# Optimization experiments

Measured on AMD Instinct MI355X. Metric: run time of the kernel, lower is better.

## Reference

```python
import jax, jax.numpy as jnp
import numpy as np

B, S, D = 32, 1024, 1024
H = 16            # attention heads
T = 8             # num_tasks (probe tokens)
E = 8             # num_experts
K = 2             # top_k
HID = 4 * D       # expert hidden dim
EPS = 1e-5


def setup_inputs() -> dict:
    key = jax.random.key(0)
    ks = jax.random.split(key, 12)
    sd = 1.0 / np.sqrt(D)
    inp = {
        "x": jax.random.normal(ks[0], (B, S, D), jnp.float32),
        "probe": jax.random.normal(ks[1], (1, T, D), jnp.float32) * 0.02,
        "in_proj_w": jax.random.normal(ks[2], (3 * D, D), jnp.float32) * sd,
        "in_proj_b": jnp.zeros((3 * D,), jnp.float32),
        "out_proj_w": jax.random.normal(ks[3], (D, D), jnp.float32) * sd,
        "out_proj_b": jnp.zeros((D,), jnp.float32),
        "ln_gamma": jnp.ones((D,), jnp.float32),
        "ln_beta": jnp.zeros((D,), jnp.float32),
        "gate_w": jax.random.normal(ks[4], (T, D, E), jnp.float32) * sd,  # per-task gate (task-aware)
        "w1": jax.random.normal(ks[5], (E, D, HID), jnp.float32) * sd,
        "b1": jnp.zeros((E, HID), jnp.float32),
        "w2": jax.random.normal(ks[6], (E, HID, D), jnp.float32) / np.sqrt(HID),
        "b2": jnp.zeros((E, D), jnp.float32),
    }
    return inp


def reference(x, probe, in_proj_w, in_proj_b, out_proj_w, out_proj_b,
              ln_gamma, ln_beta, gate_w, w1, b1, w2, b2):
    b, s, d = x.shape
    t = probe.shape[1]
    dh = d // H
    # --- multihead cross attention: query = probe, key/value = x ---
    wq, wk, wv = in_proj_w[:d], in_proj_w[d:2 * d], in_proj_w[2 * d:]
    bq, bk, bv = in_proj_b[:d], in_proj_b[d:2 * d], in_proj_b[2 * d:]
    q = jnp.broadcast_to(probe, (b, t, d)) @ wq.T + bq           # [B,T,D]
    k = x @ wk.T + bk                                            # [B,S,D]
    v = x @ wv.T + bv
    q = q.reshape(b, t, H, dh).transpose(0, 2, 1, 3)             # bhtd
    k = k.reshape(b, s, H, dh).transpose(0, 2, 1, 3)             # bhsd
    v = v.reshape(b, s, H, dh).transpose(0, 2, 1, 3)
    scores = jnp.einsum('bhtd,bhsd->bhts', q, k) / np.sqrt(dh)
    attn = jax.nn.softmax(scores, axis=-1)                       # [B,H,T,S]
    ctx = jnp.einsum('bhts,bhsd->bhtd', attn, v)
    ctx = ctx.transpose(0, 2, 1, 3).reshape(b, t, d)
    attn_out = ctx @ out_proj_w.T + out_proj_b                   # [B,T,D]
    attn_weights = attn.mean(axis=1)                             # torch avg over heads
    # --- layernorm ---
    mu = attn_out.mean(-1, keepdims=True)
    var = attn_out.var(-1, keepdims=True)
    y = (attn_out - mu) * jax.lax.rsqrt(var + EPS) * ln_gamma + ln_beta
    # --- task-aware MoE: per-task gate, top-k routing ---
    logits = jnp.einsum('btd,tde->bte', y, gate_w)               # [B,T,E]
    probs = jax.nn.softmax(logits, axis=-1)
    tok = y.reshape(b * t, d)
    p = probs.reshape(b * t, E)
    topv, topi = jax.lax.top_k(p, K)                             # [N,K]
    wgt = topv / topv.sum(-1, keepdims=True)
    gates = jnp.zeros((b * t, E), y.dtype).at[jnp.arange(b * t)[:, None], topi].set(wgt)
    # all experts on all tokens (N=B*T is small); grouped GEMM form
    h = jax.nn.gelu(jnp.einsum('nd,edh->enh', tok, w1) + b1[:, None, :], approximate=False)
    eo = jnp.einsum('enh,ehd->end', h, w2) + b2[:, None, :]      # [E,N,D]
    moe_out = jnp.einsum('ne,end->nd', gates, eo).reshape(b, t, d)
    # load-balancing aux loss
    dispatch = (jax.nn.one_hot(topi, E, dtype=y.dtype)).sum(1)   # [N,E] 0/1
    f = dispatch.mean(0)
    P = p.mean(0)
    moe_loss = E * jnp.sum(f * P)
    final = attn_out + moe_out
    return final, moe_loss, attn_weights
```

## Files before the change

kernel.cpp:

```cpp
#include <hip/hip_runtime.h>
#include <hip/hip_bf16.h>
#include <math.h>


using bf16x8  = __attribute__((ext_vector_type(8))) short;
using f32x4   = __attribute__((ext_vector_type(4))) float;
using short4v = __attribute__((ext_vector_type(4))) short;

__device__ inline short f2bf(float f) {
  unsigned u = __builtin_bit_cast(unsigned, f);
  u = (u + 0x7fffu + ((u >> 16) & 1u)) >> 16;
  return (short)u;
}
__device__ inline int bswz(int k, int n) {
  return (((k >> 3) ^ ((n >> 2) & 3)) << 3) | (k & 7);
}

#define LGKM0() asm volatile("s_waitcnt lgkmcnt(0)" ::: "memory")
#define RAWBAR() do { __builtin_amdgcn_s_barrier(); __builtin_amdgcn_sched_barrier(0); } while (0)

static constexpr long OFF_Q       = 0;
static constexpr long OFF_QWB     = 8192;
static constexpr long OFF_QB      = 73728;
static constexpr long OFF_PSUM    = 73856;
static constexpr long OFF_FCNT    = 73864;
static constexpr long OFF_GATES   = 73872;
static constexpr long OFF_CTX     = 75920;
static constexpr long OFF_ATTNOUT = 338064;
static constexpr long OFF_EO      = 600208;
static constexpr long OFF_CTXP    = 2697360;
static constexpr long OFF_AOP     = 3745936;
static constexpr long OFF_SCORES  = 4794512;
static constexpr long OFF_AXP     = 8988816;
static constexpr long OFF_YB      = 17377424;
static constexpr long OFF_HB      = 17508496;

__global__ __launch_bounds__(256) void compute_q_k(const float* __restrict__ probe,
                                                   const float* __restrict__ in_w,
                                                   const float* __restrict__ in_b,
                                                   float* __restrict__ q) {
  int wid = threadIdx.x >> 6, lane = threadIdx.x & 63;
  int idx = blockIdx.x * 4 + wid;
  int t = idx >> 10, d = idx & 1023;
  const float* pr = probe + (long)t * 1024;
  const float* wr = in_w + (long)d * 1024;
  float s = 0.f;
  for (int k = lane * 4; k < 1024; k += 256) {
    float4 a = *(const float4*)&pr[k];
    float4 b = *(const float4*)&wr[k];
    s += a.x * b.x + a.y * b.y + a.z * b.z + a.w * b.w;
  }
  for (int o = 32; o; o >>= 1) s += __shfl_xor(s, o);
  if (!lane) q[idx] = s + in_b[d];
}

__global__ __launch_bounds__(256) void compute_qw_k(const float* __restrict__ q,
                                                    const float* __restrict__ in_w,
                                                    const float* __restrict__ in_b,
                                                    short* __restrict__ qwb,
                                                    float* __restrict__ qb) {
  const int h = blockIdx.y;
  const int tid = threadIdx.x;
  const int d = blockIdx.x * 256 + tid;
  __shared__ float qh[8][64];
  if (tid < 64) {
#pragma unroll
    for (int t = 0; t < 8; ++t) qh[t][tid] = q[t * 1024 + h * 64 + tid] * 0.125f;
  }
  __syncthreads();
  const float* wk = in_w + 1048576 + (long)h * 64 * 1024;
  float acc[8];
#pragma unroll
  for (int t = 0; t < 8; ++t) acc[t] = 0.f;
  for (int j = 0; j < 64; ++j) {
    float w = wk[(long)j * 1024 + d];
#pragma unroll
    for (int t = 0; t < 8; ++t) acc[t] += qh[t][j] * w;
  }
#pragma unroll
  for (int t = 0; t < 8; ++t) qwb[(long)(h * 8 + t) * 1024 + d] = f2bf(acc[t]);
  if (blockIdx.x == 0 && tid < 8) {
    float s = 0.f;
    for (int j = 0; j < 64; ++j) s += qh[tid][j] * in_b[1024 + h * 64 + j];
    qb[h * 8 + tid] = s;
  }
}

__global__ __launch_bounds__(512)
void gemm_sc(const short* __restrict__ qwb, const float* __restrict__ xp,
             float* __restrict__ scores) {
  const int b = blockIdx.z;
  const int n0 = blockIdx.x * 64;
  const float* B = xp + (long)b * 1048576;
  float* C = scores + (long)b * 131072;
  const int tid = threadIdx.x;
  __shared__ short As[128][40], Bs[64][40];

  f32x4 acc[2][2];
#pragma unroll
  for (int i = 0; i < 2; ++i)
#pragma unroll
    for (int j = 0; j < 2; ++j)
#pragma unroll
      for (int qq = 0; qq < 4; ++qq) acc[i][j][qq] = 0.f;

  const int wid = tid >> 6, lane = tid & 63;
  const int wm = wid & 3, wn = wid >> 2;
  const int r = lane & 15, kg = (lane >> 4) * 8;
  const int am = tid >> 2, ak8 = (tid & 3) * 8;
  const int bn = tid >> 3, bk4 = (tid & 7) * 4;

  bf16x8 ra;
  float4 rb;
  auto loadT = [&](int k0) {
    ra = *(const bf16x8*)&qwb[(long)am * 1024 + k0 + ak8];
    rb = *(const float4*)&B[(long)(n0 + bn) * 1024 + k0 + bk4];
  };
  auto storeT = [&]() {
    *(bf16x8*)&As[am][ak8] = ra;
    short4v s;
    s.x = f2bf(rb.x); s.y = f2bf(rb.y); s.z = f2bf(rb.z); s.w = f2bf(rb.w);
    *(short4v*)&Bs[bn][bk4] = s;
  };
  auto compute = [&]() {
    bf16x8 af[2], bf_[2];
#pragma unroll
    for (int i = 0; i < 2; ++i) af[i] = *(const bf16x8*)&As[wm * 32 + i * 16 + r][kg];
#pragma unroll
    for (int j = 0; j < 2; ++j) bf_[j] = *(const bf16x8*)&Bs[wn * 32 + j * 16 + r][kg];
#pragma unroll
    for (int i = 0; i < 2; ++i)
#pragma unroll
      for (int j = 0; j < 2; ++j)
        acc[i][j] = __builtin_amdgcn_mfma_f32_16x16x32_bf16(af[i], bf_[j], acc[i][j], 0, 0, 0);
  };

  constexpr int NTILES = 32;
  loadT(0);
  storeT();
  loadT(32);
  LGKM0(); RAWBAR();
  for (int t = 0; t < NTILES; ++t) {
    compute();
    if (t + 1 < NTILES) {
      LGKM0(); RAWBAR();
      storeT();
      if (t + 2 < NTILES) loadT((t + 2) * 32);
      LGKM0(); RAWBAR();
    }
  }

  const int q4 = (lane >> 4) * 4;
#pragma unroll
  for (int i = 0; i < 2; ++i)
#pragma unroll
    for (int j = 0; j < 2; ++j) {
      int gn = n0 + wn * 32 + j * 16 + r;
#pragma unroll
      for (int qq = 0; qq < 4; ++qq) {
        int m = wm * 32 + i * 16 + q4 + qq;
        C[(long)m * 1024 + gn] = acc[i][j][qq];
      }
    }
}

template<int WM, int WN, int KS, bool AKB, bool BTRANS, int APL, int EPI>
__global__ __launch_bounds__(WM * WN * 64)
void gemm_ss(const float* __restrict__ Ap, const float* __restrict__ Bp,
             const float* __restrict__ kbias, float* __restrict__ Cp,
             int lda, int ldb, int K,
             long zA, long zA2, long zB, long zC, long ZKC, int ldc) {
  constexpr int BM = WM * 64, BN = WN * 64, BK = 32, NT = WM * WN * 64, PK = 40;
  constexpr int LA = BM * BK / (NT * 4), LB = BN * BK / (NT * 4);
  constexpr int F4 = BN / 4;
  const int z = blockIdx.z, zo = z / KS, kc = z % KS;
  const float* A = Ap + zA * zo + (long)kc * K;
  const float* B = BTRANS ? (Bp + zB * zo + (long)kc * K * ldb)
                          : (Bp + zB * zo + (long)kc * K);
  const float* kb = kbias + (long)kc * K;
  float* C = Cp + zC * zo + ZKC * kc;
  const int tid = threadIdx.x;
  const int m0 = blockIdx.y * BM, n0 = blockIdx.x * BN;
  __shared__ short Ah[BM][PK], Al[BM][PK], Bh[BN][PK], Bl[BN][PK];

  f32x4 acc[4][4];
#pragma unroll
  for (int i = 0; i < 4; ++i)
#pragma unroll
    for (int j = 0; j < 4; ++j)
#pragma unroll
      for (int qq = 0; qq < 4; ++qq) acc[i][j][qq] = 0.f;

  const int wid = tid >> 6, lane = tid & 63;
  const int wm = wid % WM, wn = wid / WM;
  const int r = lane & 15, kg = (lane >> 4) * 8;

  float4 ra[LA], rb[LB];

  auto loadT = [&](int k0) {
#pragma unroll
    for (int i = 0; i < LA; ++i) {
      int f = tid + i * NT;
      int m = f >> 3, k4 = (f & 7) * 4;
      long ofs = (long)(m0 + m) * lda + k0 + k4;
      ra[i] = *(const float4*)&A[ofs];
#pragma unroll
      for (int p = 1; p < APL; ++p) {
        float4 v2 = *(const float4*)&A[ofs + zA2 * p];
        ra[i].x += v2.x; ra[i].y += v2.y; ra[i].z += v2.z; ra[i].w += v2.w;
      }
      if (AKB) {
        float4 kv = *(const float4*)&kb[k0 + k4];
        ra[i].x += kv.x; ra[i].y += kv.y; ra[i].z += kv.z; ra[i].w += kv.w;
      }
    }
#pragma unroll
    for (int i = 0; i < LB; ++i) {
      int f = tid + i * NT;
      if (BTRANS) {
        int k = f / F4, n4 = (f % F4) * 4;
        rb[i] = *(const float4*)&B[(long)(k0 + k) * ldb + n0 + n4];
      } else {
        int n = f >> 3, k4 = (f & 7) * 4;
        rb[i] = *(const float4*)&B[(long)(n0 + n) * ldb + k0 + k4];
      }
    }
  };

  auto storeT = [&]() {
#pragma unroll
    for (int i = 0; i < LA; ++i) {
      int f = tid + i * NT;
      int m = f >> 3, k4 = (f & 7) * 4;
      short4v h, l;
      float vv[4] = {ra[i].x, ra[i].y, ra[i].z, ra[i].w};
#pragma unroll
      for (int j = 0; j < 4; ++j) {
        unsigned u = __builtin_bit_cast(unsigned, vv[j]);
        h[j] = (short)(u >> 16);
        l[j] = f2bf(vv[j] - __builtin_bit_cast(float, u & 0xFFFF0000u));
      }
      *(short4v*)&Ah[m][k4] = h;
      *(short4v*)&Al[m][k4] = l;
    }
#pragma unroll
    for (int i = 0; i < LB; ++i) {
      int f = tid + i * NT;
      float vv[4] = {rb[i].x, rb[i].y, rb[i].z, rb[i].w};
      if (BTRANS) {
        int k = f / F4, n4 = (f % F4) * 4;
        int col = bswz(k, n4);
#pragma unroll
        for (int j = 0; j < 4; ++j) {
          unsigned u = __builtin_bit_cast(unsigned, vv[j]);
          Bh[n4 + j][col] = (short)(u >> 16);
          Bl[n4 + j][col] = f2bf(vv[j] - __builtin_bit_cast(float, u & 0xFFFF0000u));
        }
      } else {
        int n = f >> 3, k4 = (f & 7) * 4;
        short4v h, l;
#pragma unroll
        for (int j = 0; j < 4; ++j) {
          unsigned u = __builtin_bit_cast(unsigned, vv[j]);
          h[j] = (short)(u >> 16);
          l[j] = f2bf(vv[j] - __builtin_bit_cast(float, u & 0xFFFF0000u));
        }
        *(short4v*)&Bh[n][k4] = h;
        *(short4v*)&Bl[n][k4] = l;
      }
    }
  };

  auto compute = [&]() {
    bf16x8 ah[4], al[4], bh[4], bl[4];
#pragma unroll
    for (int i = 0; i < 4; ++i) {
      ah[i] = *(const bf16x8*)&Ah[wm * 64 + i * 16 + r][kg];
      al[i] = *(const bf16x8*)&Al[wm * 64 + i * 16 + r][kg];
    }
#pragma unroll
    for (int j = 0; j < 4; ++j) {
      int brow = wn * 64 + j * 16 + r;
      int bcol = BTRANS ? bswz(kg, brow) : kg;
      bh[j] = *(const bf16x8*)&Bh[brow][bcol];
      bl[j] = *(const bf16x8*)&Bl[brow][bcol];
    }
#pragma unroll
    for (int i = 0; i < 4; ++i)
#pragma unroll
      for (int j = 0; j < 4; ++j) {
        acc[i][j] = __builtin_amdgcn_mfma_f32_16x16x32_bf16(ah[i], bh[j], acc[i][j], 0, 0, 0);
        acc[i][j] = __builtin_amdgcn_mfma_f32_16x16x32_bf16(ah[i], bl[j], acc[i][j], 0, 0, 0);
        acc[i][j] = __builtin_amdgcn_mfma_f32_16x16x32_bf16(al[i], bh[j], acc[i][j], 0, 0, 0);
      }
  };

  const int NTILES = K / BK;
  loadT(0);
  storeT();
  if (NTILES > 1) loadT(BK);
  LGKM0(); RAWBAR();
  for (int t = 0; t < NTILES; ++t) {
    compute();
    if (t + 1 < NTILES) {
      LGKM0(); RAWBAR();
      storeT();
      if (t + 2 < NTILES) loadT((t + 2) * BK);
      LGKM0(); RAWBAR();
    }
  }

  const int q4 = (lane >> 4) * 4;
#pragma unroll
  for (int i = 0; i < 4; ++i) {
    int gmb = m0 + wm * 64 + i * 16 + q4;
#pragma unroll
    for (int j = 0; j < 4; ++j) {
      int gn = n0 + wn * 64 + j * 16 + r;
#pragma unroll
      for (int qq = 0; qq < 4; ++qq) {
        float v = acc[i][j][qq];
        int m = gmb + qq;
        if constexpr (EPI == 0) {
          C[(long)m * ldc + gn] = v;
        } else {
          C[(long)(m >> 3) * 262144 + (long)(m & 7) * 1024 + gn] = v;
        }
      }
    }
  }
}

template<int WM, int WN, int KS, int EPI>
__global__ __launch_bounds__(WM * WN * 64)
void gemm_bw(const short* __restrict__ Ap, const float* __restrict__ Bp,
             const float* __restrict__ biasp, void* __restrict__ Cp,
             int lda, int ldb, int K, long zA, long zB, long zBias, long zC, int ldc) {
  constexpr int BM = WM * 64, BN = WN * 64, BK = 32, NT = WM * WN * 64, PK = 40;
  constexpr int LA = BM * BK / (NT * 8), LB = BN * BK / (NT * 4);
  constexpr int F4 = BN / 4;
  const int z = blockIdx.z, zo = z / KS, kc = z % KS;
  const short* A = Ap + zA * zo + (long)kc * K;
  const float* B = Bp + zB * zo + (long)kc * K * ldb;
  const float* bias = biasp + zBias * zo;
  const int tid = threadIdx.x;
  const int m0 = blockIdx.y * BM, n0 = blockIdx.x * BN;
  __shared__ short As[2][BM][PK], Bs[2][BN][PK];

  f32x4 acc[4][4];
#pragma unroll
  for (int i = 0; i < 4; ++i)
#pragma unroll
    for (int j = 0; j < 4; ++j)
#pragma unroll
      for (int qq = 0; qq < 4; ++qq) acc[i][j][qq] = 0.f;

  const int wid = tid >> 6, lane = tid & 63;
  const int wm = wid % WM, wn = wid / WM;
  const int r = lane & 15, kg = (lane >> 4) * 8;

  bf16x8 ra[LA];
  float4 rb[LB];

  auto loadT = [&](int k0) {
#pragma unroll
    for (int i = 0; i < LA; ++i) {
      int f = tid + i * NT;
      int m = f >> 2, k8 = (f & 3) * 8;
      ra[i] = *(const bf16x8*)&A[(long)(m0 + m) * lda + k0 + k8];
    }
#pragma unroll
    for (int i = 0; i < LB; ++i) {
      int f = tid + i * NT;
      int k = f / F4, n4 = (f % F4) * 4;
      rb[i] = *(const float4*)&B[(long)(k0 + k) * ldb + n0 + n4];
    }
  };

  auto storeT = [&](int bi) {
#pragma unroll
    for (int i = 0; i < LA; ++i) {
      int f = tid + i * NT;
      int m = f >> 2, k8 = (f & 3) * 8;
      *(bf16x8*)&As[bi][m][k8] = ra[i];
    }
#pragma unroll
    for (int i = 0; i < LB; ++i) {
      int f = tid + i * NT;
      int k = f / F4, n4 = (f % F4) * 4;
      int col = bswz(k, n4);
      Bs[bi][n4 + 0][col] = f2bf(rb[i].x);
      Bs[bi][n4 + 1][col] = f2bf(rb[i].y);
      Bs[bi][n4 + 2][col] = f2bf(rb[i].z);
      Bs[bi][n4 + 3][col] = f2bf(rb[i].w);
    }
  };

  auto compute = [&](int bi) {
    bf16x8 af[4], bfr[4];
#pragma unroll
    for (int i = 0; i < 4; ++i) af[i] = *(const bf16x8*)&As[bi][wm * 64 + i * 16 + r][kg];
#pragma unroll
    for (int j = 0; j < 4; ++j) {
      int brow = wn * 64 + j * 16 + r;
      bfr[j] = *(const bf16x8*)&Bs[bi][brow][bswz(kg, brow)];
    }
#pragma unroll
    for (int i = 0; i < 4; ++i)
#pragma unroll
      for (int j = 0; j < 4; ++j)
        acc[i][j] = __builtin_amdgcn_mfma_f32_16x16x32_bf16(af[i], bfr[j], acc[i][j], 0, 0, 0);
  };

  const int NTILES = K / BK;
  loadT(0);
  storeT(0);
  if (NTILES > 1) loadT(BK);
  LGKM0(); RAWBAR();
  for (int t = 0; t < NTILES; ++t) {
    compute(t & 1);
    if (t + 1 < NTILES) {
      storeT((t + 1) & 1);
      if (t + 2 < NTILES) loadT((t + 2) * BK);
      LGKM0(); RAWBAR();
    }
  }

  const int q4 = (lane >> 4) * 4;
#pragma unroll
  for (int i = 0; i < 4; ++i) {
    int gmb = m0 + wm * 64 + i * 16 + q4;
#pragma unroll
    for (int j = 0; j < 4; ++j) {
      int gn = n0 + wn * 64 + j * 16 + r;
#pragma unroll
      for (int qq = 0; qq < 4; ++qq) {
        float v = acc[i][j][qq];
        int m = gmb + qq;
        if constexpr (EPI == 2) {
          float u = v + bias[gn];
          u = 0.5f * u * (1.0f + erff(u * 0.70710678118654752f));
          ((short*)Cp + zC * zo)[(long)m * ldc + gn] = f2bf(u);
        } else {
          atomicAdd(&((float*)Cp + zC * zo)[(long)m * ldc + gn], v);
        }
      }
    }
  }
}

__global__ __launch_bounds__(256) void reduce4_k(const float* __restrict__ p,
                                                 float* __restrict__ out) {
  int i = (blockIdx.x * 256 + threadIdx.x) * 4;
  float4 a = *(const float4*)&p[i];
  float4 b = *(const float4*)&p[i + 262144];
  float4 c = *(const float4*)&p[i + 524288];
  float4 d = *(const float4*)&p[i + 786432];
  float4 o;
  o.x = a.x + b.x + c.x + d.x;
  o.y = a.y + b.y + c.y + d.y;
  o.z = a.z + b.z + c.z + d.z;
  o.w = a.w + b.w + c.w + d.w;
  *(float4*)&out[i] = o;
}

__global__ __launch_bounds__(256) void softmax_k(float* __restrict__ scores,
                                                 const float* __restrict__ qb) {
  long row = blockIdx.x;
  float bias = qb[(int)(row & 127)];
  float* p = scores + row * 1024;
  int tid = threadIdx.x;
  int wid = tid >> 6, lane = tid & 63;
  float v[4];
  float mx = -1e30f;
#pragma unroll
  for (int i = 0; i < 4; ++i) {
    v[i] = p[tid + i * 256] + bias;
    mx = fmaxf(mx, v[i]);
  }
  for (int o = 32; o; o >>= 1) mx = fmaxf(mx, __shfl_xor(mx, o));
  __shared__ float sm[4];
  __shared__ float ss[4];
  if (!lane) sm[wid] = mx;
  __syncthreads();
  mx = fmaxf(fmaxf(sm[0], sm[1]), fmaxf(sm[2], sm[3]));
  float s = 0.f;
#pragma unroll
  for (int i = 0; i < 4; ++i) { v[i] = expf(v[i] - mx); s += v[i]; }
  for (int o = 32; o; o >>= 1) s += __shfl_xor(s, o);
  if (!lane) ss[wid] = s;
  __syncthreads();
  s = ss[0] + ss[1] + ss[2] + ss[3];
  float inv = 1.0f / s;
#pragma unroll
  for (int i = 0; i < 4; ++i) p[tid + i * 256] = v[i] * inv;
}

__global__ __launch_bounds__(256) void attnw_k(const float* __restrict__ attn,
                                               float* __restrict__ outw) {
  int idx = blockIdx.x * 256 + threadIdx.x;
  int b = idx >> 13;
  int r = idx & 8191;
  int t = r >> 10, s = r & 1023;
  const float* p = attn + (long)b * 131072 + (long)t * 1024 + s;
  float acc = 0.f;
#pragma unroll
  for (int h = 0; h < 16; ++h) acc += p[(long)h * 8192];
  outw[idx] = acc * (1.0f / 16.0f);
}

__global__ __launch_bounds__(256) void ln_gate_k(const float* __restrict__ aop,
                                                 const float* __restrict__ out_b,
                                                 const float* __restrict__ gamma,
                                                 const float* __restrict__ beta,
                                                 const float* __restrict__ gate_w,
                                                 float* __restrict__ attn_out,
                                                 short* __restrict__ yb,
                                                 float* __restrict__ gates,
                                                 float* __restrict__ Psum,
                                                 float* __restrict__ fcnt) {
  int row = blockIdx.x;
  int t = row & 7;
  int tid = threadIdx.x;
  int wid = tid >> 6, lane = tid & 63;
  const float* xr = aop + (long)row * 1024;
  float vals[4];
  float s = 0.f, sq = 0.f;
#pragma unroll
  for (int i = 0; i < 4; ++i) {
    int d = tid + i * 256;
    float v = xr[d] + xr[d + 262144] + xr[d + 524288] + xr[d + 786432] + out_b[d];
    attn_out[(long)row * 1024 + d] = v;
    vals[i] = v;
    s += v;
    sq += v * v;
  }
  for (int o = 32; o; o >>= 1) { s += __shfl_xor(s, o); sq += __shfl_xor(sq, o); }
  __shared__ float rs[4], rss[4];
  if (!lane) { rs[wid] = s; rss[wid] = sq; }
  __syncthreads();
  s = rs[0] + rs[1] + rs[2] + rs[3];
  sq = rss[0] + rss[1] + rss[2] + rss[3];
  float mu = s * (1.0f / 1024.0f);
  float var = sq * (1.0f / 1024.0f) - mu * mu;
  float rstd = rsqrtf(var + 1e-5f);
  __shared__ float yrow[1024];
#pragma unroll
  for (int i = 0; i < 4; ++i) {
    int d = tid + i * 256;
    float yv = (vals[i] - mu) * rstd * gamma[d] + beta[d];
    yb[(long)row * 1024 + d] = f2bf(yv);
    yrow[d] = yv;
  }
  __syncthreads();
  int e = tid & 7;
  int g = tid >> 3;
  float acc = 0.f;
  const float* gw = gate_w + (long)t * 8192;
  for (int d = g; d < 1024; d += 32) acc += yrow[d] * gw[d * 8 + e];
  __shared__ float part[256];
  __shared__ float lsh[8];
  part[tid] = acc;
  __syncthreads();
  if (tid < 8) {
    float l = 0.f;
    for (int gg = 0; gg < 32; ++gg) l += part[gg * 8 + tid];
    lsh[tid] = l;
  }
  __syncthreads();
  if (tid == 0) {
    float p[8];
    float mx = -1e30f;
    for (int k = 0; k < 8; ++k) mx = fmaxf(mx, lsh[k]);
    float sum = 0.f;
    for (int k = 0; k < 8; ++k) { p[k] = expf(lsh[k] - mx); sum += p[k]; }
    float inv = 1.0f / sum;
    for (int k = 0; k < 8; ++k) p[k] *= inv;
    int i0 = 0;
    for (int k = 1; k < 8; ++k) if (p[k] > p[i0]) i0 = k;
    int i1 = -1;
    for (int k = 0; k < 8; ++k) if (k != i0 && (i1 < 0 || p[k] > p[i1])) i1 = k;
    float tot = p[i0] + p[i1];
    for (int k = 0; k < 8; ++k)
      gates[(long)row * 8 + k] = (k == i0) ? p[i0] / tot : (k == i1) ? p[i1] / tot : 0.f;
    for (int k = 0; k < 8; ++k) atomicAdd(&Psum[k], p[k]);
    atomicAdd(&fcnt[i0], 1.0f);
    atomicAdd(&fcnt[i1], 1.0f);
  }
}

__global__ __launch_bounds__(256) void combine_k(const float* __restrict__ attn_out,
                                                 const float* __restrict__ eo,
                                                 const float* __restrict__ b2,
                                                 const float* __restrict__ gates,
                                                 float* __restrict__ outp) {
  int idx = blockIdx.x * 256 + threadIdx.x;
  int n = idx >> 10, d = idx & 1023;
  float v = attn_out[idx];
  const float* g = gates + (long)n * 8;
#pragma unroll
  for (int e = 0; e < 8; ++e) {
    float ge = g[e];
    if (ge != 0.f) v += ge * (eo[(long)e * 262144 + idx] + b2[e * 1024 + d]);
  }
  outp[idx] = v;
}

__global__ void loss_k(const float* __restrict__ Psum, const float* __restrict__ fcnt,
                       float* __restrict__ out) {
  if (threadIdx.x == 0) {
    float l = 0.f;
    for (int e = 0; e < 8; ++e) l += (fcnt[e] * (1.0f / 256.0f)) * (Psum[e] * (1.0f / 256.0f));
    out[0] = 8.0f * l;
  }
}

extern "C" void kernel_launch(void* const* d_in, const int* in_sizes, int n_in,
                              void* d_out, int out_size, void* d_ws, size_t ws_size,
                              hipStream_t stream) {
  const float* x      = (const float*)d_in[0];
  const float* probe  = (const float*)d_in[1];
  const float* in_w   = (const float*)d_in[2];
  const float* in_b   = (const float*)d_in[3];
  const float* out_w  = (const float*)d_in[4];
  const float* out_b  = (const float*)d_in[5];
  const float* gamma  = (const float*)d_in[6];
  const float* beta   = (const float*)d_in[7];
  const float* gate_w = (const float*)d_in[8];
  const float* w1     = (const float*)d_in[9];
  const float* b1     = (const float*)d_in[10];
  const float* w2     = (const float*)d_in[11];
  const float* b2     = (const float*)d_in[12];

  float* ws = (float*)d_ws;
  float* q        = ws + OFF_Q;
  short* qwb      = (short*)(ws + OFF_QWB);
  float* qb       = ws + OFF_QB;
  float* Psum     = ws + OFF_PSUM;
  float* fcnt     = ws + OFF_FCNT;
  float* gates    = ws + OFF_GATES;
  float* ctx      = ws + OFF_CTX;
  float* attn_out = ws + OFF_ATTNOUT;
  float* eo       = ws + OFF_EO;
  float* ctxp     = ws + OFF_CTXP;
  float* aop      = ws + OFF_AOP;
  float* scores   = ws + OFF_SCORES;
  float* axp      = ws + OFF_AXP;
  short* yb       = (short*)(ws + OFF_YB);
  short* hb       = (short*)(ws + OFF_HB);

  float* out_final = (float*)d_out;
  float* out_loss  = out_final + 262144;
  float* out_attnw = out_loss + 1;

  hipMemsetAsync(ws + OFF_PSUM, 0, 16 * sizeof(float), stream);
  hipMemsetAsync(eo, 0, 2097152 * sizeof(float), stream);

  compute_q_k<<<2048, 256, 0, stream>>>(probe, in_w, in_b, q);
  compute_qw_k<<<dim3(4, 16, 1), 256, 0, stream>>>(q, in_w, in_b, qwb, qb);

  gemm_sc<<<dim3(16, 1, 32), 512, 0, stream>>>(qwb, x, scores);

  softmax_k<<<4096, 256, 0, stream>>>(scores, qb);
  attnw_k<<<1024, 256, 0, stream>>>(scores, out_attnw);

  gemm_ss<2, 2, 2, false, true, 1, 4><<<dim3(8, 1, 64), 256, 0, stream>>>(
      scores, x, qb , axp, 1024, 1024, 512,
      131072L, 0L, 1048576L, 8192L, 4194304L, 1024);

  gemm_ss<1, 1, 4, false, false, 2, 0><<<dim3(1, 4, 64), 64, 0, stream>>>(
      axp, in_w + 2097152, qb , ctxp, 1024, 1024, 256,
      262144L, 4194304L, 65536L, 64L, 262144L, 1024);
  reduce4_k<<<256, 256, 0, stream>>>(ctxp, ctx);

  gemm_ss<1, 1, 4, true, false, 1, 0><<<dim3(16, 4, 4), 64, 0, stream>>>(
      ctx, out_w, in_b + 2048, aop, 1024, 1024, 256,
      0L, 0L, 0L, 0L, 262144L, 1024);

  ln_gate_k<<<256, 256, 0, stream>>>(aop, out_b, gamma, beta, gate_w, attn_out,
                                     yb, gates, Psum, fcnt);

  gemm_bw<2, 2, 1, 2><<<dim3(32, 2, 8), 256, 0, stream>>>(
      yb, w1, b1, hb, 1024, 4096, 1024, 0L, 4194304L, 4096L, 1048576L, 4096);

  gemm_bw<2, 2, 4, 5><<<dim3(8, 2, 32), 256, 0, stream>>>(
      hb, w2, b2 , eo, 4096, 1024, 1024, 1048576L, 4194304L, 0L, 262144L, 1024);

  combine_k<<<1024, 256, 0, stream>>>(attn_out, eo, b2, gates, out_final);
  loss_k<<<1, 64, 0, stream>>>(Psum, fcnt, out_loss);
}
```

Measured before the change: 364.8 us.

## Retile MoE expert GEMMs and replace split-K atomics with partial buffers

The expert GEMM kernel now uses a fixed 128x64 tile with BK=64, two waves per block and a single LDS buffer, where it had a configurable 2x2-wave, double-buffered BK=32 tile. The split-K second GEMM writes each K-chunk into its own partial buffer instead of using atomicAdd. The combine kernel sums the four partials, which removes the memset of the expert output. This trades atomic traffic and a memset for a larger workspace and extra reads in combine. Losing double buffering adds an extra barrier per K tile.

```diff
diff --git a/kernel.cpp b/kernel.cpp
--- a/kernel.cpp
+++ b/kernel.cpp
@@ -27,13 +27,13 @@
 static constexpr long OFF_GATES   = 73872;
 static constexpr long OFF_CTX     = 75920;
 static constexpr long OFF_ATTNOUT = 338064;
-static constexpr long OFF_EO      = 600208;
-static constexpr long OFF_CTXP    = 2697360;
-static constexpr long OFF_AOP     = 3745936;
-static constexpr long OFF_SCORES  = 4794512;
-static constexpr long OFF_AXP     = 8988816;
-static constexpr long OFF_YB      = 17377424;
-static constexpr long OFF_HB      = 17508496;
+static constexpr long OFF_EOP     = 600208;
+static constexpr long OFF_CTXP    = 8988816;
+static constexpr long OFF_AOP     = 10037392;
+static constexpr long OFF_SCORES  = 11085968;
+static constexpr long OFF_AXP     = 15280272;
+static constexpr long OFF_YB      = 23668880;
+static constexpr long OFF_HB      = 23799952;
 
 __global__ __launch_bounds__(256) void compute_q_k(const float* __restrict__ probe,
                                                    const float* __restrict__ in_w,
@@ -331,13 +331,14 @@
   }
 }
 
-template<int WM, int WN, int KS, int EPI>
-__global__ __launch_bounds__(WM * WN * 64)
+template<int KS, int EPI>
+__global__ __launch_bounds__(128)
 void gemm_bw(const short* __restrict__ Ap, const float* __restrict__ Bp,
              const float* __restrict__ biasp, void* __restrict__ Cp,
-             int lda, int ldb, int K, long zA, long zB, long zBias, long zC, int ldc) {
-  constexpr int BM = WM * 64, BN = WN * 64, BK = 32, NT = WM * WN * 64, PK = 40;
-  constexpr int LA = BM * BK / (NT * 8), LB = BN * BK / (NT * 4);
+             int lda, int ldb, int K, long zA, long zB, long zBias, long zC, long ZKC, int ldc) {
+  constexpr int BM = 128, BN = 64, BK = 64, NT = 128, PK = 72;
+  constexpr int LA = BM * BK / (NT * 8);
+  constexpr int LB = BN * BK / (NT * 4);
   constexpr int F4 = BN / 4;
   const int z = blockIdx.z, zo = z / KS, kc = z % KS;
   const short* A = Ap + zA * zo + (long)kc * K;
@@ -345,7 +346,7 @@
   const float* bias = biasp + zBias * zo;
   const int tid = threadIdx.x;
   const int m0 = blockIdx.y * BM, n0 = blockIdx.x * BN;
-  __shared__ short As[2][BM][PK], Bs[2][BN][PK];
+  __shared__ short As[BM][PK], Bs[BN][PK];
 
   f32x4 acc[4][4];
 #pragma unroll
@@ -356,7 +357,7 @@
       for (int qq = 0; qq < 4; ++qq) acc[i][j][qq] = 0.f;
 
   const int wid = tid >> 6, lane = tid & 63;
-  const int wm = wid % WM, wn = wid / WM;
+  const int wm = wid;
   const int r = lane & 15, kg = (lane >> 4) * 8;
 
   bf16x8 ra[LA];
@@ -366,7 +367,7 @@
 #pragma unroll
     for (int i = 0; i < LA; ++i) {
       int f = tid + i * NT;
-      int m = f >> 2, k8 = (f & 3) * 8;
+      int m = f >> 3, k8 = (f & 7) * 8;
       ra[i] = *(const bf16x8*)&A[(long)(m0 + m) * lda + k0 + k8];
     }
 #pragma unroll
@@ -377,50 +378,55 @@
     }
   };
 
-  auto storeT = [&](int bi) {
+  auto storeT = [&]() {
 #pragma unroll
     for (int i = 0; i < LA; ++i) {
       int f = tid + i * NT;
-      int m = f >> 2, k8 = (f & 3) * 8;
-      *(bf16x8*)&As[bi][m][k8] = ra[i];
+      int m = f >> 3, k8 = (f & 7) * 8;
+      *(bf16x8*)&As[m][k8] = ra[i];
     }
 #pragma unroll
     for (int i = 0; i < LB; ++i) {
       int f = tid + i * NT;
       int k = f / F4, n4 = (f % F4) * 4;
       int col = bswz(k, n4);
-      Bs[bi][n4 + 0][col] = f2bf(rb[i].x);
-      Bs[bi][n4 + 1][col] = f2bf(rb[i].y);
-      Bs[bi][n4 + 2][col] = f2bf(rb[i].z);
-      Bs[bi][n4 + 3][col] = f2bf(rb[i].w);
-    }
-  };
-
-  auto compute = [&](int bi) {
-    bf16x8 af[4], bfr[4];
-#pragma unroll
-    for (int i = 0; i < 4; ++i) af[i] = *(const bf16x8*)&As[bi][wm * 64 + i * 16 + r][kg];
-#pragma unroll
-    for (int j = 0; j < 4; ++j) {
-      int brow = wn * 64 + j * 16 + r;
-      bfr[j] = *(const bf16x8*)&Bs[bi][brow][bswz(kg, brow)];
-    }
-#pragma unroll
-    for (int i = 0; i < 4; ++i)
-#pragma unroll
-      for (int j = 0; j < 4; ++j)
-        acc[i][j] = __builtin_amdgcn_mfma_f32_16x16x32_bf16(af[i], bfr[j], acc[i][j], 0, 0, 0);
+      Bs[n4 + 0][col] = f2bf(rb[i].x);
+      Bs[n4 + 1][col] = f2bf(rb[i].y);
+      Bs[n4 + 2][col] = f2bf(rb[i].z);
+      Bs[n4 + 3][col] = f2bf(rb[i].w);
+    }
+  };
+
+  auto compute = [&]() {
+#pragma unroll
+    for (int kk = 0; kk < 2; ++kk) {
+      bf16x8 af[4], bfr[4];
+#pragma unroll
+      for (int i = 0; i < 4; ++i)
+        af[i] = *(const bf16x8*)&As[wm * 64 + i * 16 + r][kk * 32 + kg];
+#pragma unroll
+      for (int j = 0; j < 4; ++j) {
+        int brow = j * 16 + r;
+        bfr[j] = *(const bf16x8*)&Bs[brow][bswz(kk * 32 + kg, brow)];
+      }
+#pragma unroll
+      for (int i = 0; i < 4; ++i)
+#pragma unroll
+        for (int j = 0; j < 4; ++j)
+          acc[i][j] = __builtin_amdgcn_mfma_f32_16x16x32_bf16(af[i], bfr[j], acc[i][j], 0, 0, 0);
+    }
   };
 
   const int NTILES = K / BK;
   loadT(0);
-  storeT(0);
+  storeT();
   if (NTILES > 1) loadT(BK);
   LGKM0(); RAWBAR();
   for (int t = 0; t < NTILES; ++t) {
-    compute(t & 1);
+    compute();
     if (t + 1 < NTILES) {
-      storeT((t + 1) & 1);
+      LGKM0(); RAWBAR();
+      storeT();
       if (t + 2 < NTILES) loadT((t + 2) * BK);
       LGKM0(); RAWBAR();
     }
@@ -432,7 +438,7 @@
     int gmb = m0 + wm * 64 + i * 16 + q4;
 #pragma unroll
     for (int j = 0; j < 4; ++j) {
-      int gn = n0 + wn * 64 + j * 16 + r;
+      int gn = n0 + j * 16 + r;
 #pragma unroll
       for (int qq = 0; qq < 4; ++qq) {
         float v = acc[i][j][qq];
@@ -442,7 +448,7 @@
           u = 0.5f * u * (1.0f + erff(u * 0.70710678118654752f));
           ((short*)Cp + zC * zo)[(long)m * ldc + gn] = f2bf(u);
         } else {
-          atomicAdd(&((float*)Cp + zC * zo)[(long)m * ldc + gn], v);
+          ((float*)Cp + zC * zo + ZKC * kc)[(long)m * ldc + gn] = v;
         }
       }
     }
@@ -590,7 +596,7 @@
 }
 
 __global__ __launch_bounds__(256) void combine_k(const float* __restrict__ attn_out,
-                                                 const float* __restrict__ eo,
+                                                 const float* __restrict__ eop,
                                                  const float* __restrict__ b2,
                                                  const float* __restrict__ gates,
                                                  float* __restrict__ outp) {
@@ -601,7 +607,11 @@
 #pragma unroll
   for (int e = 0; e < 8; ++e) {
     float ge = g[e];
-    if (ge != 0.f) v += ge * (eo[(long)e * 262144 + idx] + b2[e * 1024 + d]);
+    if (ge != 0.f) {
+      long base = (long)e * 262144 + idx;
+      float s = eop[base] + eop[base + 2097152] + eop[base + 4194304] + eop[base + 6291456];
+      v += ge * (s + b2[e * 1024 + d]);
+    }
   }
   outp[idx] = v;
 }
@@ -641,7 +651,7 @@
   float* gates    = ws + OFF_GATES;
   float* ctx      = ws + OFF_CTX;
   float* attn_out = ws + OFF_ATTNOUT;
-  float* eo       = ws + OFF_EO;
+  float* eop      = ws + OFF_EOP;
   float* ctxp     = ws + OFF_CTXP;
   float* aop      = ws + OFF_AOP;
   float* scores   = ws + OFF_SCORES;
@@ -654,7 +664,6 @@
   float* out_attnw = out_loss + 1;
 
   hipMemsetAsync(ws + OFF_PSUM, 0, 16 * sizeof(float), stream);
-  hipMemsetAsync(eo, 0, 2097152 * sizeof(float), stream);
 
   compute_q_k<<<2048, 256, 0, stream>>>(probe, in_w, in_b, q);
   compute_qw_k<<<dim3(4, 16, 1), 256, 0, stream>>>(q, in_w, in_b, qwb, qb);
@@ -680,12 +689,12 @@
   ln_gate_k<<<256, 256, 0, stream>>>(aop, out_b, gamma, beta, gate_w, attn_out,
                                      yb, gates, Psum, fcnt);
 
-  gemm_bw<2, 2, 1, 2><<<dim3(32, 2, 8), 256, 0, stream>>>(
-      yb, w1, b1, hb, 1024, 4096, 1024, 0L, 4194304L, 4096L, 1048576L, 4096);
-
-  gemm_bw<2, 2, 4, 5><<<dim3(8, 2, 32), 256, 0, stream>>>(
-      hb, w2, b2 , eo, 4096, 1024, 1024, 1048576L, 4194304L, 0L, 262144L, 1024);
-
-  combine_k<<<1024, 256, 0, stream>>>(attn_out, eo, b2, gates, out_final);
+  gemm_bw<1, 2><<<dim3(64, 2, 8), 128, 0, stream>>>(
+      yb, w1, b1, hb, 1024, 4096, 1024, 0L, 4194304L, 4096L, 1048576L, 0L, 4096);
+
+  gemm_bw<4, 5><<<dim3(16, 2, 32), 128, 0, stream>>>(
+      hb, w2, b2 , eop, 4096, 1024, 1024, 1048576L, 4194304L, 0L, 262144L, 2097152L, 1024);
+
+  combine_k<<<1024, 256, 0, stream>>>(attn_out, eop, b2, gates, out_final);
   loss_k<<<1, 64, 0, stream>>>(Psum, fcnt, out_loss);
 }
```

Result: faster. 352.8 us (-3.3%).
